# Kernel tuning notes

Hardware: AMD Instinct MI355X
Metric: run time of the kernel (lower is better)

Reference implementation:

```python
import jax, jax.numpy as jnp
import numpy as np

NUM_CEPS = 13  # default num_ceps in log_mel_to_cepstral


def _dct_basis(n_mels, num_ceps):
    # Orthonormal DCT-II basis (scipy.fftpack.dct type=2, norm='ortho'),
    # truncated to the first num_ceps rows. Shape (num_ceps, n_mels).
    n = jnp.arange(n_mels, dtype=jnp.float32)
    k = jnp.arange(num_ceps, dtype=jnp.float32)
    basis = jnp.cos(jnp.pi * (n[None, :] + 0.5) * k[:, None] / n_mels)
    scale = jnp.where(k == 0, jnp.sqrt(1.0 / n_mels), jnp.sqrt(2.0 / n_mels))
    return basis * scale[:, None]


def _log_mel_to_cepstral(mel, basis):
    # mel: (B, 1, F, T) -> cepstral (B, num_ceps, T) with CMVN over (B*T)
    x = jnp.log1p(jnp.abs(mel[:, 0]))                 # (B, F, T)
    c = jnp.einsum('kf,bft->bkt', basis, x)           # (B, num_ceps, T)
    mean = jnp.mean(c, axis=(0, 2), keepdims=True)
    # torch .std is unbiased (ddof=1) over the B*T flattened samples
    std = jnp.std(c, axis=(0, 2), keepdims=True, ddof=1) + 1e-6
    return (c - mean) / std


def setup_inputs() -> dict:
    key = jax.random.key(0)
    k1, k2 = jax.random.split(key)
    B, F, T = 64, 128, 4096
    mel_true = jax.random.normal(k1, (B, 1, F, T), dtype=jnp.float32)
    mel_pred = jax.random.normal(k2, (B, 1, F, T), dtype=jnp.float32)
    return {"mel_true": mel_true, "mel_pred": mel_pred}


def reference(mel_true, mel_pred):
    n_mels = mel_true.shape[2]
    basis = _dct_basis(n_mels, NUM_CEPS)
    c_true = _log_mel_to_cepstral(mel_true, basis)
    c_pred = _log_mel_to_cepstral(mel_pred, basis)
    diff = c_true - c_pred
    mse_dist = jnp.sum(diff * diff, axis=1)           # (B, T)
    log_base_10 = 10.0 / jnp.log(jnp.float32(10.0))
    mcd = log_base_10 * jnp.sqrt(2.0 * mse_dist)
    return jnp.mean(mcd)
```

## Files before the change

kernel.cpp:

```cpp
#include <hip/hip_runtime.h>
#include <math.h>

#define BB 64
#define FF 128
#define TT 4096
#define KK 13
#define NT (BB * TT)
#define NPAIR (NT / 2)
#define MCD_C  6.14185100f



#define KLIST(X) X(0) X(1) X(2) X(3) X(4) X(5) X(6) X(7) X(8) X(9) X(10) X(11) X(12)
#define K12(X)        X(1) X(2) X(3) X(4) X(5) X(6) X(7) X(8) X(9) X(10) X(11) X(12)

__global__ __launch_bounds__(256)
__attribute__((amdgpu_waves_per_eu(4, 4)))
void pass1_kernel(
    const float* __restrict__ melT, const float* __restrict__ melP,
    float* __restrict__ sums, float* __restrict__ cT, float* __restrict__ cP)
{
    const int tensor = blockIdx.x >> 9;
    const int gp = ((blockIdx.x & 511) << 8) + threadIdx.x;
    const float* __restrict__ src = tensor ? melP : melT;
    float* __restrict__ dst = tensor ? cP : cT;

    const int g0 = gp << 1;
    const int b  = g0 >> 12;
    const int t0 = g0 & (TT - 1);
    const float* p = src + (size_t)b * (FF * TT) + t0;

#define DECLACC(i) float ax##i = 0.f, ay##i = 0.f;
    KLIST(DECLACC)
#undef DECLACC

    for (int f0 = 0; f0 < FF; f0 += 8) {
        float2 v[8];
#pragma unroll
        for (int j = 0; j < 8; ++j)
            v[j] = *(const float2*)(p + (size_t)(f0 + j) * TT);

#pragma unroll
        for (int j = 0; j < 8; ++j) {
            const float xx = __log2f(1.0f + fabsf(v[j].x));
            const float xy = __log2f(1.0f + fabsf(v[j].y));

            const float b1 = __cosf((3.14159265358979f / 128.0f) *
                                    ((float)(f0 + j) + 0.5f));
            const float tw = b1 + b1;
            const float b2  = fmaf(tw, b1,  -1.0f);
            const float b3  = fmaf(tw, b2,  -b1);
            const float b4  = fmaf(tw, b3,  -b2);
            const float b5  = fmaf(tw, b4,  -b3);
            const float b6  = fmaf(tw, b5,  -b4);
            const float b7  = fmaf(tw, b6,  -b5);
            const float b8  = fmaf(tw, b7,  -b6);
            const float b9  = fmaf(tw, b8,  -b7);
            const float b10 = fmaf(tw, b9,  -b8);
            const float b11 = fmaf(tw, b10, -b9);
            const float b12 = fmaf(tw, b11, -b10);

            ax0 += xx; ay0 += xy;
#define FMAK(i) ax##i = fmaf(b##i, xx, ax##i); ay##i = fmaf(b##i, xy, ay##i);
            K12(FMAK)
#undef FMAK
        }
    }

#define STK(i) ((float2*)(dst + (size_t)(i) * NT))[gp] = make_float2(ax##i, ay##i);
    KLIST(STK)
#undef STK

    __shared__ float red[4][26];
    const int lane = threadIdx.x & 63;
    const int wave = threadIdx.x >> 6;
#define REDK(i) { \
        float s = ax##i + ay##i; \
        float q = fmaf(ax##i, ax##i, ay##i * ay##i); \
        for (int o = 32; o > 0; o >>= 1) { \
            s += __shfl_down(s, o); q += __shfl_down(q, o); } \
        if (lane == 0) { red[wave][i] = s; red[wave][13 + i] = q; } }
    KLIST(REDK)
#undef REDK
    __syncthreads();
    if (threadIdx.x < 26) {
        const float v = red[0][threadIdx.x] + red[1][threadIdx.x] +
                        red[2][threadIdx.x] + red[3][threadIdx.x];
        atomicAdd(&sums[(tensor * 26 + threadIdx.x) * 16], v);
    }
}

__global__ __launch_bounds__(256, 4) void pass2_kernel(
    const float* __restrict__ sums, const float* __restrict__ cT,
    const float* __restrict__ cP, float* __restrict__ partials)
{
    __shared__ float mT[13], iT[13], mP[13], iP[13];
    if (threadIdx.x < 26) {
        const int tns = threadIdx.x >= 13;
        const int k   = threadIdx.x - tns * 13;
        const float s = sums[(tns * 26 + k) * 16];
        const float q = sums[(tns * 26 + 13 + k) * 16];
        const float N = (float)NT;
        const float m = s / N;
        const float var = fmaxf((q - s * m) / (N - 1.0f), 0.0f);
        const float isd = 1.0f / (sqrtf(var) + 1e-6f);
        if (tns == 0) { mT[k] = m; iT[k] = isd; }
        else          { mP[k] = m; iP[k] = isd; }
    }
    __syncthreads();

    const int gp = blockIdx.x * 256 + threadIdx.x;
    float ssx = 0.0f, ssy = 0.0f;
#pragma unroll
    for (int k = 0; k < KK; ++k) {
        const float2 a = ((const float2*)(cT + (size_t)k * NT))[gp];
        const float2 p = ((const float2*)(cP + (size_t)k * NT))[gp];
        const float dx = (a.x - mT[k]) * iT[k] - (p.x - mP[k]) * iP[k];
        const float dy = (a.y - mT[k]) * iT[k] - (p.y - mP[k]) * iP[k];
        ssx = fmaf(dx, dx, ssx);
        ssy = fmaf(dy, dy, ssy);
    }
    float v = MCD_C * (sqrtf(ssx) + sqrtf(ssy));

    const int lane = threadIdx.x & 63;
    const int wave = threadIdx.x >> 6;
    for (int o = 32; o > 0; o >>= 1) v += __shfl_down(v, o);
    __shared__ float r2[4];
    if (lane == 0) r2[wave] = v;
    __syncthreads();
    if (threadIdx.x == 0)
        partials[blockIdx.x] = r2[0] + r2[1] + r2[2] + r2[3];
}

__global__ __launch_bounds__(256) void pass3_kernel(
    const float* __restrict__ partials, float* __restrict__ out)
{
    float v = partials[threadIdx.x] + partials[threadIdx.x + 256];
    const int lane = threadIdx.x & 63;
    const int wave = threadIdx.x >> 6;
    for (int o = 32; o > 0; o >>= 1) v += __shfl_down(v, o);
    __shared__ float r2[4];
    if (lane == 0) r2[wave] = v;
    __syncthreads();
    if (threadIdx.x == 0)
        out[0] = (r2[0] + r2[1] + r2[2] + r2[3]) * (1.0f / (float)NT);
}

extern "C" void kernel_launch(void* const* d_in, const int* in_sizes, int n_in,
                              void* d_out, int out_size, void* d_ws, size_t ws_size,
                              hipStream_t stream) {
    const float* melT = (const float*)d_in[0];
    const float* melP = (const float*)d_in[1];
    float* out      = (float*)d_out;
    float* sums     = (float*)d_ws;
    float* partials = (float*)((char*)d_ws + 4096);
    float* cT       = (float*)((char*)d_ws + 8192);
    float* cP       = cT + (size_t)KK * NT;

    hipMemsetAsync(d_ws, 0, 4096, stream);

    pass1_kernel<<<1024, 256, 0, stream>>>(melT, melP, sums, cT, cP);
    pass2_kernel<<<512, 256, 0, stream>>>(sums, cT, cP, partials);
    pass3_kernel<<<1, 256, 0, stream>>>(partials, out);
}
```

Measured before the change: 287.4 us.

## Exploit DCT basis symmetry to halve FMAs and use one time step per thread

The DCT-II basis is symmetric for even k and antisymmetric for odd k, so the pass-1 kernel pairs mel bins f and F-1-f and accumulates their sum or difference. This halves the number of basis FMAs. Each thread now handles one time sample instead of two, doubling the grid and raising the waves-per-EU hint to 8, so occupancy goes up while the loads become scalar 4-byte accesses instead of float2. Pass 2 and pass 3 are adjusted to the new per-element layout and the larger partials array. The memset is widened to cover the larger partials buffer.

New measurement: 299.8 us. 1.04x slower.

```diff
diff --git a/kernel.cpp b/kernel.cpp
--- a/kernel.cpp
+++ b/kernel.cpp
@@ -6,68 +6,69 @@
 #define TT 4096
 #define KK 13
 #define NT (BB * TT)
-#define NPAIR (NT / 2)
 #define MCD_C  6.14185100f
 
 
 
 #define KLIST(X) X(0) X(1) X(2) X(3) X(4) X(5) X(6) X(7) X(8) X(9) X(10) X(11) X(12)
-#define K12(X)        X(1) X(2) X(3) X(4) X(5) X(6) X(7) X(8) X(9) X(10) X(11) X(12)
 
 __global__ __launch_bounds__(256)
-__attribute__((amdgpu_waves_per_eu(4, 4)))
+__attribute__((amdgpu_waves_per_eu(8)))
 void pass1_kernel(
     const float* __restrict__ melT, const float* __restrict__ melP,
     float* __restrict__ sums, float* __restrict__ cT, float* __restrict__ cP)
 {
-    const int tensor = blockIdx.x >> 9;
-    const int gp = ((blockIdx.x & 511) << 8) + threadIdx.x;
+    const int tensor = blockIdx.x >> 10;
+    const int g = ((blockIdx.x & 1023) << 8) + threadIdx.x;
     const float* __restrict__ src = tensor ? melP : melT;
     float* __restrict__ dst = tensor ? cP : cT;
 
-    const int g0 = gp << 1;
-    const int b  = g0 >> 12;
-    const int t0 = g0 & (TT - 1);
-    const float* p = src + (size_t)b * (FF * TT) + t0;
+    const int b = g >> 12;
+    const int t = g & (TT - 1);
+    const float* p = src + (size_t)b * (FF * TT) + t;
 
-#define DECLACC(i) float ax##i = 0.f, ay##i = 0.f;
+#define DECLACC(i) float a##i = 0.f;
     KLIST(DECLACC)
 #undef DECLACC
 
-    for (int f0 = 0; f0 < FF; f0 += 8) {
-        float2 v[8];
+    for (int f0 = 0; f0 < FF / 2; f0 += 8) {
+        float xa[8], xb[8];
 #pragma unroll
         for (int j = 0; j < 8; ++j)
-            v[j] = *(const float2*)(p + (size_t)(f0 + j) * TT);
+            xa[j] = p[(size_t)(f0 + j) * TT];
+#pragma unroll
+        for (int j = 0; j < 8; ++j)
+            xb[j] = p[(size_t)(FF - 1 - f0 - j) * TT];
 
 #pragma unroll
         for (int j = 0; j < 8; ++j) {
-            const float xx = __log2f(1.0f + fabsf(v[j].x));
-            const float xy = __log2f(1.0f + fabsf(v[j].y));
-
-            const float b1 = __cosf((3.14159265358979f / 128.0f) *
+            const float x1 = __log2f(1.0f + fabsf(xa[j]));
+            const float x2 = __log2f(1.0f + fabsf(xb[j]));
+            const float s = x1 + x2;
+            const float d = x1 - x2;
+            const float c1 = __cosf((3.14159265358979f / 128.0f) *
                                     ((float)(f0 + j) + 0.5f));
-            const float tw = b1 + b1;
-            const float b2  = fmaf(tw, b1,  -1.0f);
-            const float b3  = fmaf(tw, b2,  -b1);
-            const float b4  = fmaf(tw, b3,  -b2);
-            const float b5  = fmaf(tw, b4,  -b3);
-            const float b6  = fmaf(tw, b5,  -b4);
-            const float b7  = fmaf(tw, b6,  -b5);
-            const float b8  = fmaf(tw, b7,  -b6);
-            const float b9  = fmaf(tw, b8,  -b7);
-            const float b10 = fmaf(tw, b9,  -b8);
-            const float b11 = fmaf(tw, b10, -b9);
-            const float b12 = fmaf(tw, b11, -b10);
-
-            ax0 += xx; ay0 += xy;
-#define FMAK(i) ax##i = fmaf(b##i, xx, ax##i); ay##i = fmaf(b##i, xy, ay##i);
-            K12(FMAK)
-#undef FMAK
+            const float tw = c1 + c1;
+            float bp = 1.0f, bc = c1;
+            a0 += s;
+#define ROLL { const float bn = fmaf(tw, bc, -bp); bp = bc; bc = bn; }
+            a1  = fmaf(bc, d, a1);  ROLL
+            a2  = fmaf(bc, s, a2);  ROLL
+            a3  = fmaf(bc, d, a3);  ROLL
+            a4  = fmaf(bc, s, a4);  ROLL
+            a5  = fmaf(bc, d, a5);  ROLL
+            a6  = fmaf(bc, s, a6);  ROLL
+            a7  = fmaf(bc, d, a7);  ROLL
+            a8  = fmaf(bc, s, a8);  ROLL
+            a9  = fmaf(bc, d, a9);  ROLL
+            a10 = fmaf(bc, s, a10); ROLL
+            a11 = fmaf(bc, d, a11); ROLL
+            a12 = fmaf(bc, s, a12);
+#undef ROLL
         }
     }
 
-#define STK(i) ((float2*)(dst + (size_t)(i) * NT))[gp] = make_float2(ax##i, ay##i);
+#define STK(i) dst[(size_t)(i) * NT + g] = a##i;
     KLIST(STK)
 #undef STK
 
@@ -75,8 +76,8 @@
     const int lane = threadIdx.x & 63;
     const int wave = threadIdx.x >> 6;
 #define REDK(i) { \
-        float s = ax##i + ay##i; \
-        float q = fmaf(ax##i, ax##i, ay##i * ay##i); \
+        float s = a##i; \
+        float q = a##i * a##i; \
         for (int o = 32; o > 0; o >>= 1) { \
             s += __shfl_down(s, o); q += __shfl_down(q, o); } \
         if (lane == 0) { red[wave][i] = s; red[wave][13 + i] = q; } }
@@ -90,7 +91,7 @@
     }
 }
 
-__global__ __launch_bounds__(256, 4) void pass2_kernel(
+__global__ __launch_bounds__(256) void pass2_kernel(
     const float* __restrict__ sums, const float* __restrict__ cT,
     const float* __restrict__ cP, float* __restrict__ partials)
 {
@@ -109,18 +110,20 @@
     }
     __syncthreads();
 
-    const int gp = blockIdx.x * 256 + threadIdx.x;
-    float ssx = 0.0f, ssy = 0.0f;
+    const int g = blockIdx.x * 256 + threadIdx.x;
+    float vT[KK], vP[KK];
+#pragma unroll
+    for (int k = 0; k < KK; ++k) vT[k] = cT[(size_t)k * NT + g];
+#pragma unroll
+    for (int k = 0; k < KK; ++k) vP[k] = cP[(size_t)k * NT + g];
+
+    float ss = 0.0f;
 #pragma unroll
     for (int k = 0; k < KK; ++k) {
-        const float2 a = ((const float2*)(cT + (size_t)k * NT))[gp];
-        const float2 p = ((const float2*)(cP + (size_t)k * NT))[gp];
-        const float dx = (a.x - mT[k]) * iT[k] - (p.x - mP[k]) * iP[k];
-        const float dy = (a.y - mT[k]) * iT[k] - (p.y - mP[k]) * iP[k];
-        ssx = fmaf(dx, dx, ssx);
-        ssy = fmaf(dy, dy, ssy);
+        const float d = (vT[k] - mT[k]) * iT[k] - (vP[k] - mP[k]) * iP[k];
+        ss = fmaf(d, d, ss);
     }
-    float v = MCD_C * (sqrtf(ssx) + sqrtf(ssy));
+    float v = MCD_C * sqrtf(ss);
 
     const int lane = threadIdx.x & 63;
     const int wave = threadIdx.x >> 6;
@@ -135,7 +138,8 @@
 __global__ __launch_bounds__(256) void pass3_kernel(
     const float* __restrict__ partials, float* __restrict__ out)
 {
-    float v = partials[threadIdx.x] + partials[threadIdx.x + 256];
+    float v = partials[threadIdx.x] + partials[threadIdx.x + 256] +
+              partials[threadIdx.x + 512] + partials[threadIdx.x + 768];
     const int lane = threadIdx.x & 63;
     const int wave = threadIdx.x >> 6;
     for (int o = 32; o > 0; o >>= 1) v += __shfl_down(v, o);
@@ -157,9 +161,9 @@
     float* cT       = (float*)((char*)d_ws + 8192);
     float* cP       = cT + (size_t)KK * NT;
 
-    hipMemsetAsync(d_ws, 0, 4096, stream);
+    hipMemsetAsync(d_ws, 0, 8192, stream);
 
-    pass1_kernel<<<1024, 256, 0, stream>>>(melT, melP, sums, cT, cP);
-    pass2_kernel<<<512, 256, 0, stream>>>(sums, cT, cP, partials);
+    pass1_kernel<<<2048, 256, 0, stream>>>(melT, melP, sums, cT, cP);
+    pass2_kernel<<<1024, 256, 0, stream>>>(sums, cT, cP, partials);
     pass3_kernel<<<1, 256, 0, stream>>>(partials, out);
 }
```
